# Kernel tuning notes

Hardware: AMD Instinct MI355X
Metric: run time of the kernel (lower is better)

The kernel has to match this reference:

```python
import jax, jax.numpy as jnp
import numpy as np
from jax import lax

D_MODEL = 512
D_STATE = 16
D_CONV = 4
EXPAND = 2
D_INNER = EXPAND * D_MODEL          # 1024
DT_RANK = int(np.ceil(D_MODEL / 16))  # 32


def setup_inputs() -> dict:
    key = jax.random.key(0)
    ks = jax.random.split(key, 10)
    s = lambda k, shape, sc: (jax.random.normal(k, shape, dtype=jnp.float32) * sc)
    x = jax.random.normal(ks[0], (8, D_MODEL, 128, 128), dtype=jnp.float32)
    W_in = s(ks[1], (2 * D_INNER, D_MODEL), 1.0 / np.sqrt(D_MODEL))
    conv_w = s(ks[2], (D_INNER, D_CONV), 1.0 / np.sqrt(D_CONV))
    conv_b = s(ks[3], (D_INNER,), 0.02)
    W_x = s(ks[4], (DT_RANK + 2 * D_STATE, D_INNER), 1.0 / np.sqrt(D_INNER))
    W_dt = s(ks[5], (D_INNER, DT_RANK), 1.0 / np.sqrt(DT_RANK))
    b_dt = s(ks[6], (D_INNER,), 0.02)
    # S4D-real init: A_log[d, n] = log(n+1)
    A_log = jnp.log(jnp.broadcast_to(jnp.arange(1, D_STATE + 1, dtype=jnp.float32), (D_INNER, D_STATE)))
    D_param = jnp.ones((D_INNER,), dtype=jnp.float32)
    W_out = s(ks[7], (D_MODEL, D_INNER), 1.0 / np.sqrt(D_INNER))
    return {"x": x, "W_in": W_in, "conv_w": conv_w, "conv_b": conv_b,
            "W_x": W_x, "W_dt": W_dt, "b_dt": b_dt, "A_log": A_log,
            "D_param": D_param, "W_out": W_out}


def _mamba(u, W_in, conv_w, conv_b, W_x, W_dt, b_dt, A_log, D_param, W_out):
    # u: (B, L, D_MODEL)
    B, L, _ = u.shape
    xz = jnp.einsum('bld,ed->ble', u, W_in)          # (B, L, 2*D_INNER)
    xp, z = jnp.split(xz, 2, axis=-1)                # each (B, L, D_INNER)
    # causal depthwise conv1d over L
    xc = lax.conv_general_dilated(
        xp.transpose(0, 2, 1), conv_w[:, None, :],
        window_strides=(1,), padding=((D_CONV - 1, 0),),
        dimension_numbers=('NCH', 'OIH', 'NCH'),
        feature_group_count=D_INNER)
    xc = xc[:, :, :L] + conv_b[None, :, None]
    xs = jax.nn.silu(xc.transpose(0, 2, 1))          # (B, L, D_INNER)
    x_dbl = jnp.einsum('bld,ed->ble', xs, W_x)       # (B, L, DT_RANK+2*D_STATE)
    dt, Bm, Cm = jnp.split(x_dbl, [DT_RANK, DT_RANK + D_STATE], axis=-1)
    delta = jax.nn.softplus(jnp.einsum('blr,dr->bld', dt, W_dt) + b_dt)  # (B,L,D_INNER)
    A = -jnp.exp(A_log)                              # (D_INNER, D_STATE)
    dA = jnp.exp(jnp.einsum('bld,dn->bldn', delta, A))
    dBx = jnp.einsum('bld,bln,bld->bldn', delta, Bm, xs)

    def step(h, inp):
        dA_t, dBx_t, C_t = inp
        h = dA_t * h + dBx_t                         # (B, D_INNER, D_STATE)
        y = jnp.einsum('bdn,bn->bd', h, C_t)
        return h, y

    h0 = jnp.zeros((B, D_INNER, D_STATE), dtype=u.dtype)
    _, ys = lax.scan(step, h0, (dA.transpose(1, 0, 2, 3),
                                dBx.transpose(1, 0, 2, 3),
                                Cm.transpose(1, 0, 2)))
    y = ys.transpose(1, 0, 2)                        # (B, L, D_INNER)
    y = y + D_param * xs
    y = y * jax.nn.silu(z)
    return jnp.einsum('bld,ed->ble', y, W_out)       # (B, L, D_MODEL)


def reference(x, W_in, conv_w, conv_b, W_x, W_dt, b_dt, A_log, D_param, W_out):
    # ECA: global avg pool -> (B, 1, C) sequence through Mamba -> sigmoid gate
    y = jnp.mean(x, axis=(2, 3))[:, None, :]         # (B, 1, C)
    y = _mamba(y, W_in, conv_w, conv_b, W_x, W_dt, b_dt, A_log, D_param, W_out)
    gate = jax.nn.sigmoid(y)[:, 0, :, None, None]    # (B, C, 1, 1)
    return x * gate
```

## Files before the change

### kernel.cpp

```cpp
#include <hip/hip_runtime.h>
#include <math.h>

#define DMODEL 512
#define DINNER 1024
#define DTRANK 32
#define DSTATE 16
#define HW     16384
#define BATCH  8

typedef float vf4 __attribute__((ext_vector_type(4)));

__device__ __forceinline__ float wave_reduce(float s) {
#pragma unroll
    for (int off = 32; off; off >>= 1) s += __shfl_xor(s, off);
    return s;
}

__global__ __launch_bounds__(256) void mean_kernel(const float* __restrict__ x,
                                                   float* __restrict__ mean_out) {
    const int row = blockIdx.x;
    const vf4* xr = (const vf4*)(x + (size_t)row * HW);
    const int t = threadIdx.x;
    float s = 0.f;
#pragma unroll
    for (int j = 0; j < 16; ++j) {
        vf4 v = xr[t + j * 256];
        s += v.x + v.y + v.z + v.w;
    }
    for (int off = 32; off; off >>= 1) s += __shfl_down(s, off);
    __shared__ float part[4];
    if ((t & 63) == 0) part[t >> 6] = s;
    __syncthreads();
    if (t == 0) {
        float tot = part[0] + part[1] + part[2] + part[3];
        mean_out[row] = tot * (1.0f / (float)HW);
    }
}

__global__ __launch_bounds__(256) void k2a_win_kernel(
    const float* __restrict__ mean_in,
    const float* __restrict__ W_in,
    const float* __restrict__ conv_w,
    const float* __restrict__ conv_b,
    float* __restrict__ xs_buf,
    float* __restrict__ sz_buf)
{
    __shared__ float u[BATCH * DMODEL];
    const int t = threadIdx.x;
#pragma unroll
    for (int i = 0; i < 16; ++i) u[t + i * 256] = mean_in[t + i * 256];
    __syncthreads();

    const int wave = blockIdx.x * 4 + (t >> 6);
    const int lane = t & 63;
    const vf4* row = (const vf4*)(W_in + (size_t)wave * DMODEL);
    const vf4 w0 = row[lane];
    const vf4 w1 = row[lane + 64];
    const vf4* u4 = (const vf4*)u;

    float acc[BATCH];
#pragma unroll
    for (int b = 0; b < BATCH; ++b) {
        vf4 a = u4[b * 128 + lane];
        vf4 c = u4[b * 128 + lane + 64];
        acc[b] = w0.x * a.x + w0.y * a.y + w0.z * a.z + w0.w * a.w
               + w1.x * c.x + w1.y * c.y + w1.z * c.z + w1.w * c.w;
    }
#pragma unroll
    for (int b = 0; b < BATCH; ++b) acc[b] = wave_reduce(acc[b]);

    if (lane == 0) {
        if (wave < DINNER) {
            const float cw = conv_w[wave * 4 + 3];
            const float cb = conv_b[wave];
#pragma unroll
            for (int b = 0; b < BATCH; ++b) {
                float xc = acc[b] * cw + cb;
                xs_buf[b * DINNER + wave] = xc / (1.f + expf(-xc));
            }
        } else {
            const int d = wave - DINNER;
#pragma unroll
            for (int b = 0; b < BATCH; ++b) {
                float zc = acc[b];
                sz_buf[b * DINNER + d] = zc / (1.f + expf(-zc));
            }
        }
    }
}

__global__ __launch_bounds__(256) void k2b_mid_kernel(
    const float* __restrict__ xs_buf,
    const float* __restrict__ sz_buf,
    const float* __restrict__ W_x,
    const float* __restrict__ W_dt,
    const float* __restrict__ b_dt,
    const float* __restrict__ D_param,
    float* __restrict__ yv_buf)
{
    __shared__ float xs[DINNER];
    __shared__ float xdbl[64];
    const int b = blockIdx.x;
    const int t = threadIdx.x;
    const int lane = t & 63;
    const int wv = t >> 6;

#pragma unroll
    for (int i = 0; i < 4; ++i) xs[t + i * 256] = xs_buf[b * DINNER + t + i * 256];
    __syncthreads();

    const vf4* xs4 = (const vf4*)xs;
    for (int oi = 0; oi < 16; ++oi) {
        const int o = wv * 16 + oi;
        const vf4* wr = (const vf4*)(W_x + (size_t)o * DINNER);
        float acc = 0.f;
#pragma unroll
        for (int j = 0; j < 4; ++j) {
            vf4 w = wr[lane + j * 64];
            vf4 v = xs4[lane + j * 64];
            acc += w.x * v.x + w.y * v.y + w.z * v.z + w.w * v.w;
        }
        acc = wave_reduce(acc);
        if (lane == 0) xdbl[o] = acc;
    }
    __syncthreads();

    float bc = 0.f;
#pragma unroll
    for (int n = 0; n < DSTATE; ++n)
        bc += xdbl[DTRANK + n] * xdbl[DTRANK + DSTATE + n];

#pragma unroll
    for (int k = 0; k < 4; ++k) {
        const int d = t + k * 256;
        float acc = b_dt[d];
        const vf4* wr = (const vf4*)(W_dt + (size_t)d * DTRANK);
        const vf4* dt4 = (const vf4*)xdbl;
#pragma unroll
        for (int r = 0; r < 8; ++r) {
            vf4 w = wr[r]; vf4 v = dt4[r];
            acc += w.x * v.x + w.y * v.y + w.z * v.z + w.w * v.w;
        }
        float delta = (acc > 20.f) ? acc : log1pf(expf(acc));
        yv_buf[b * DINNER + d] =
            (delta * bc + D_param[d]) * xs[d] * sz_buf[b * DINNER + d];
    }
}

__global__ __launch_bounds__(256) void k2c_wout_kernel(
    const float* __restrict__ yv_buf,
    const float* __restrict__ W_out,
    float* __restrict__ gate_out)
{
    __shared__ float yv[BATCH * DINNER];
    const int t = threadIdx.x;
#pragma unroll
    for (int i = 0; i < 32; ++i) yv[t + i * 256] = yv_buf[t + i * 256];
    __syncthreads();

    const int wave = blockIdx.x * 4 + (t >> 6);
    const int lane = t & 63;
    const vf4* row = (const vf4*)(W_out + (size_t)wave * DINNER);
    const vf4* yv4 = (const vf4*)yv;

    float acc[BATCH];
#pragma unroll
    for (int b = 0; b < BATCH; ++b) acc[b] = 0.f;
#pragma unroll
    for (int j = 0; j < 4; ++j) {
        vf4 w = row[lane + j * 64];
#pragma unroll
        for (int b = 0; b < BATCH; ++b) {
            vf4 v = yv4[b * 256 + lane + j * 64];
            acc[b] += w.x * v.x + w.y * v.y + w.z * v.z + w.w * v.w;
        }
    }
#pragma unroll
    for (int b = 0; b < BATCH; ++b) acc[b] = wave_reduce(acc[b]);

    if (lane == 0) {
#pragma unroll
        for (int b = 0; b < BATCH; ++b)
            gate_out[b * DMODEL + wave] = 1.f / (1.f + expf(-acc[b]));
    }
}

__global__ __launch_bounds__(256) void gate_mul_kernel(const float* __restrict__ x,
                                                       const float* __restrict__ gate,
                                                       float* __restrict__ out) {
    const int row = blockIdx.x;
    const float g = gate[row];
    const vf4* xi = (const vf4*)(x + (size_t)row * HW);
    vf4* oo = (vf4*)(out + (size_t)row * HW);
    const int t = threadIdx.x;
#pragma unroll
    for (int j = 0; j < 16; ++j) {
        vf4 v = xi[t + j * 256];
        v *= g;
        __builtin_nontemporal_store(v, &oo[t + j * 256]);
    }
}

extern "C" void kernel_launch(void* const* d_in, const int* in_sizes, int n_in,
                              void* d_out, int out_size, void* d_ws, size_t ws_size,
                              hipStream_t stream) {
    const float* x       = (const float*)d_in[0];
    const float* W_in    = (const float*)d_in[1];
    const float* conv_w  = (const float*)d_in[2];
    const float* conv_b  = (const float*)d_in[3];
    const float* W_x     = (const float*)d_in[4];
    const float* W_dt    = (const float*)d_in[5];
    const float* b_dt    = (const float*)d_in[6];
    const float* D_param = (const float*)d_in[8];
    const float* W_out   = (const float*)d_in[9];
    float* out = (float*)d_out;

    float* mean_buf = (float*)d_ws;
    float* gate_buf = mean_buf + BATCH * DMODEL;
    float* xs_buf   = gate_buf + BATCH * DMODEL;
    float* sz_buf   = xs_buf + BATCH * DINNER;
    float* yv_buf   = sz_buf + BATCH * DINNER;

    mean_kernel<<<BATCH * DMODEL, 256, 0, stream>>>(x, mean_buf);
    k2a_win_kernel<<<512, 256, 0, stream>>>(mean_buf, W_in, conv_w, conv_b,
                                            xs_buf, sz_buf);
    k2b_mid_kernel<<<BATCH, 256, 0, stream>>>(xs_buf, sz_buf, W_x, W_dt, b_dt,
                                              D_param, yv_buf);
    k2c_wout_kernel<<<128, 256, 0, stream>>>(yv_buf, W_out, gate_buf);
    gate_mul_kernel<<<BATCH * DMODEL, 256, 0, stream>>>(x, gate_buf, out);
}
```

Measured before the change: 152.9 us.

## Fuse W_out projection and sigmoid gate into the gate-multiply kernel

Removes the separate W_out GEMV kernel. Each gate-multiply block now computes its own channel's gate with a one-wave dot product over the 1024-wide yv row, overlapped with prefetching its 64KB x slice into registers. Rows are processed in reverse order so recently read x data is more likely still resident in cache from the mean pass. This saves one launch and the gate buffer round trip, at the cost of redundant dot products (four waves each compute the same one) and higher register pressure.

```diff
diff --git a/kernel.cpp b/kernel.cpp
--- a/kernel.cpp
+++ b/kernel.cpp
@@ -147,57 +147,41 @@
     }
 }
 
-__global__ __launch_bounds__(256) void k2c_wout_kernel(
+__global__ __launch_bounds__(256) void gate_mul_kernel(
+    const float* __restrict__ x,
     const float* __restrict__ yv_buf,
     const float* __restrict__ W_out,
-    float* __restrict__ gate_out)
+    float* __restrict__ out)
 {
-    __shared__ float yv[BATCH * DINNER];
-    const int t = threadIdx.x;
-#pragma unroll
-    for (int i = 0; i < 32; ++i) yv[t + i * 256] = yv_buf[t + i * 256];
-    __syncthreads();
-
-    const int wave = blockIdx.x * 4 + (t >> 6);
+    const int row = (BATCH * DMODEL - 1) - blockIdx.x;
+    const int b = row >> 9;
+    const int c = row & 511;
+    const int t = threadIdx.x;
     const int lane = t & 63;
-    const vf4* row = (const vf4*)(W_out + (size_t)wave * DINNER);
-    const vf4* yv4 = (const vf4*)yv;
-
-    float acc[BATCH];
-#pragma unroll
-    for (int b = 0; b < BATCH; ++b) acc[b] = 0.f;
-#pragma unroll
-    for (int j = 0; j < 4; ++j) {
-        vf4 w = row[lane + j * 64];
-#pragma unroll
-        for (int b = 0; b < BATCH; ++b) {
-            vf4 v = yv4[b * 256 + lane + j * 64];
-            acc[b] += w.x * v.x + w.y * v.y + w.z * v.z + w.w * v.w;
-        }
-    }
-#pragma unroll
-    for (int b = 0; b < BATCH; ++b) acc[b] = wave_reduce(acc[b]);
-
-    if (lane == 0) {
-#pragma unroll
-        for (int b = 0; b < BATCH; ++b)
-            gate_out[b * DMODEL + wave] = 1.f / (1.f + expf(-acc[b]));
-    }
-}
-
-__global__ __launch_bounds__(256) void gate_mul_kernel(const float* __restrict__ x,
-                                                       const float* __restrict__ gate,
-                                                       float* __restrict__ out) {
-    const int row = blockIdx.x;
-    const float g = gate[row];
+
+    const vf4* wr = (const vf4*)(W_out + (size_t)c * DINNER);
+    const vf4* yv = (const vf4*)(yv_buf + (size_t)b * DINNER);
+    vf4 w[4], y[4];
+#pragma unroll
+    for (int j = 0; j < 4; ++j) { w[j] = wr[lane + j * 64]; y[j] = yv[lane + j * 64]; }
+
     const vf4* xi = (const vf4*)(x + (size_t)row * HW);
     vf4* oo = (vf4*)(out + (size_t)row * HW);
-    const int t = threadIdx.x;
+    vf4 v[16];
+#pragma unroll
+    for (int j = 0; j < 16; ++j) v[j] = xi[t + j * 256];
+
+    float acc = 0.f;
+#pragma unroll
+    for (int j = 0; j < 4; ++j)
+        acc += w[j].x * y[j].x + w[j].y * y[j].y + w[j].z * y[j].z + w[j].w * y[j].w;
+    acc = wave_reduce(acc);
+    const float g = 1.f / (1.f + expf(-acc));
+
 #pragma unroll
     for (int j = 0; j < 16; ++j) {
-        vf4 v = xi[t + j * 256];
-        v *= g;
-        __builtin_nontemporal_store(v, &oo[t + j * 256]);
+        vf4 o = v[j] * g;
+        __builtin_nontemporal_store(o, &oo[t + j * 256]);
     }
 }
 
@@ -216,8 +200,7 @@
     float* out = (float*)d_out;
 
     float* mean_buf = (float*)d_ws;
-    float* gate_buf = mean_buf + BATCH * DMODEL;
-    float* xs_buf   = gate_buf + BATCH * DMODEL;
+    float* xs_buf   = mean_buf + BATCH * DMODEL;
     float* sz_buf   = xs_buf + BATCH * DINNER;
     float* yv_buf   = sz_buf + BATCH * DINNER;
 
@@ -226,6 +209,5 @@
                                             xs_buf, sz_buf);
     k2b_mid_kernel<<<BATCH, 256, 0, stream>>>(xs_buf, sz_buf, W_x, W_dt, b_dt,
                                               D_param, yv_buf);
-    k2c_wout_kernel<<<128, 256, 0, stream>>>(yv_buf, W_out, gate_buf);
-    gate_mul_kernel<<<BATCH * DMODEL, 256, 0, stream>>>(x, gate_buf, out);
-}
+    gate_mul_kernel<<<BATCH * DMODEL, 256, 0, stream>>>(x, yv_buf, W_out, out);
+}
```

New measurement: 149.0 us. 2.5% less time.
